# Kernel optimization log

Measured on AMD Instinct MI355X. Metric: run time of the kernel, lower is better.

Reference implementation:

```python
import jax, jax.numpy as jnp
import numpy as np

D_MODEL = 1024
HEADS = 16
Q_DIM = 1024
HEAD_DIM = Q_DIM // HEADS


def setup_inputs() -> dict:
    key = jax.random.key(0)
    ks = jax.random.split(key, 9)
    B, S = 2, 2048
    scale = 1.0 / np.sqrt(D_MODEL)
    inp = {
        "embeddings": jax.random.normal(ks[0], (B, S, D_MODEL), dtype=jnp.float32),
        "Wq": jax.random.normal(ks[1], (D_MODEL, Q_DIM), dtype=jnp.float32) * scale,
        "bq": jnp.zeros((Q_DIM,), dtype=jnp.float32),
        "Wk": jax.random.normal(ks[2], (D_MODEL, Q_DIM), dtype=jnp.float32) * scale,
        "bk": jnp.zeros((Q_DIM,), dtype=jnp.float32),
        "Wv": jax.random.normal(ks[3], (D_MODEL, Q_DIM), dtype=jnp.float32) * scale,
        "bv": jnp.zeros((Q_DIM,), dtype=jnp.float32),
        "Wo": jax.random.normal(ks[4], (Q_DIM, D_MODEL), dtype=jnp.float32) * scale,
        "bo": jnp.zeros((D_MODEL,), dtype=jnp.float32),
    }
    return inp


def reference(embeddings, Wq, bq, Wk, bk, Wv, bv, Wo, bo):
    B, S, _ = embeddings.shape
    # projections -> [B, H, S, Dh]
    def proj(W, b):
        x = embeddings @ W + b
        return x.reshape(B, S, HEADS, HEAD_DIM).transpose(0, 2, 1, 3)
    q = proj(Wq, bq)
    k = proj(Wk, bk)
    v = proj(Wv, bv)
    # scores scaled by sqrt(head_dim) as in source (no mask, dropout is no-op)
    scores = jnp.einsum("bhqd,bhkd->bhqk", q, k) / jnp.sqrt(
        jnp.asarray(HEAD_DIM, dtype=q.dtype)
    )
    p = jax.nn.softmax(scores, axis=-1)
    attn = jnp.einsum("bhqk,bhkd->bhqd", p, v)
    attn = attn.transpose(0, 2, 1, 3).reshape(B, S, Q_DIM)
    return attn @ Wo + bo
```

## Files before the change

kernel.cpp:

```cpp
#include <hip/hip_runtime.h>
#include <hip/hip_bf16.h>

#define BB 2
#define SS 2048
#define DMODEL 1024
#define NHEADS 16
#define DHEAD 64
#define MTOT (BB*SS)
#define NQKV 3072
#define QSCALE 0.18033688011112042f

typedef short bh8 __attribute__((ext_vector_type(8)));
typedef float fx4 __attribute__((ext_vector_type(4)));
typedef unsigned int ux2 __attribute__((ext_vector_type(2)));

__device__ __forceinline__ short f2bs(float f) {
    __hip_bfloat16 h = __float2bfloat16(f);
    return *reinterpret_cast<short*>(&h);
}

__device__ __forceinline__ unsigned pk_bf16(float a, float b) {
    __hip_bfloat162 h = __float22bfloat162_rn(make_float2(a, b));
    return *reinterpret_cast<unsigned*>(&h);
}

__device__ __forceinline__ void gload_lds16(const short* g, short* l) {
    __builtin_amdgcn_global_load_lds(
        (const __attribute__((address_space(1))) unsigned int*)g,
        (__attribute__((address_space(3))) unsigned int*)l, 16, 0, 0);
}

__global__ __launch_bounds__(256) void cvt_emb(const float* __restrict__ x,
                                               short* __restrict__ y, int n) {
    int i = (blockIdx.x * 256 + threadIdx.x) * 4;
    if (i + 3 < n) {
        float4 v = *(const float4*)(x + i);
        short4 o;
        o.x = f2bs(v.x); o.y = f2bs(v.y); o.z = f2bs(v.z); o.w = f2bs(v.w);
        *(short4*)(y + i) = o;
    }
}

__global__ __launch_bounds__(256) void transpose_w(
        const float* __restrict__ Wq, const float* __restrict__ Wk,
        const float* __restrict__ Wv, const float* __restrict__ Wo,
        short* __restrict__ Wt_qkv, short* __restrict__ Wot) {
    __shared__ float tile[64][65];
    int z = blockIdx.z;
    const float* src = (z == 0) ? Wq : (z == 1) ? Wk : (z == 2) ? Wv : Wo;
    short* dst = (z == 3) ? Wot : (Wt_qkv + (size_t)z * 1024 * 1024);
    int n0 = blockIdx.x * 64, k0 = blockIdx.y * 64;
    int tx = threadIdx.x, ty = threadIdx.y;
    for (int j = 0; j < 16; j++) {
        int r = ty + j * 4;
        tile[r][tx] = src[(size_t)(k0 + r) * 1024 + n0 + tx];
    }
    __syncthreads();
    for (int j = 0; j < 16; j++) {
        int r = ty + j * 4;
        dst[(size_t)(n0 + r) * 1024 + k0 + tx] = f2bs(tile[tx][r]);
    }
}

template<int BM, int BN, int NN, int MODE>
__global__ __launch_bounds__(256) void gemm_bt_t(
        const short* __restrict__ A, const short* __restrict__ Bt,
        const float* __restrict__ bq, const float* __restrict__ bk,
        const float* __restrict__ bv, const float* __restrict__ bo,
        short* __restrict__ Qout, short* __restrict__ Kout,
        short* __restrict__ Vtout, float* __restrict__ Cout) {
    const int K = 1024;
    constexpr int ROWS = BM + BN;
    constexpr int CPW  = ROWS / 64;
    constexpr int MBK  = MTOT / BM;
    constexpr int STRIP = MBK / 8;
    constexpr int MT = BM / 32, NT = BN / 32;
    __shared__ __align__(16) short S[3][ROWS * 32];

    int tid = threadIdx.x;
    int w = tid >> 6, l = tid & 63, quad = l >> 4, ln = l & 15;
    int wm = w & 1, wn = w >> 1;

    int id = blockIdx.x;
    int xcd = id & 7, local = id >> 3;
    int mi = xcd * STRIP + (local % STRIP);
    int ni = local / STRIP;
    int m0 = mi * BM, n0 = ni * BN;

    const short* gsrc[CPW];
    int loff[CPW];
    #pragma unroll
    for (int j = 0; j < CPW; j++) {
        int r0 = (w * CPW + j) * 16;
        int row = r0 + (l >> 2);
        gsrc[j] = (r0 < BM ? A + (size_t)(m0 + row) * K
                           : Bt + (size_t)(n0 + row - BM) * K) + (l & 3) * 8;
        loff[j] = r0 * 32;
    }

    short *sC = &S[0][0], *sN = &S[1][0], *sN2 = &S[2][0];
    #pragma unroll
    for (int j = 0; j < CPW; j++) gload_lds16(gsrc[j], sC + loff[j]);
    #pragma unroll
    for (int j = 0; j < CPW; j++) gload_lds16(gsrc[j] + 32, sN + loff[j]);

    fx4 acc[MT][NT] = {};
    for (int it = 0; it < 32; ++it) {
        if (it < 31) {
            if constexpr (CPW == 4)
                asm volatile("s_waitcnt vmcnt(4)\n\ts_barrier" ::: "memory");
            else
                asm volatile("s_waitcnt vmcnt(3)\n\ts_barrier" ::: "memory");
        } else {
            asm volatile("s_waitcnt vmcnt(0)\n\ts_barrier" ::: "memory");
        }
        if (it < 30) {
            int k0 = (it + 2) * 32;
            #pragma unroll
            for (int j = 0; j < CPW; j++) gload_lds16(gsrc[j] + k0, sN2 + loff[j]);
        }
        bh8 af[MT], bf[NT];
        #pragma unroll
        for (int mt = 0; mt < MT; mt++)
            af[mt] = *(const bh8*)&sC[(wm * (BM / 2) + mt * 16 + ln) * 32 + quad * 8];
        #pragma unroll
        for (int nt = 0; nt < NT; nt++)
            bf[nt] = *(const bh8*)&sC[(BM + wn * (BN / 2) + nt * 16 + ln) * 32 + quad * 8];
        #pragma unroll
        for (int mt = 0; mt < MT; mt++)
            #pragma unroll
            for (int nt = 0; nt < NT; nt++)
                acc[mt][nt] = __builtin_amdgcn_mfma_f32_16x16x32_bf16(af[mt], bf[nt], acc[mt][nt], 0, 0, 0);
        short* t;
        t = sC; sC = sN; sN = sN2; sN2 = t;
    }

    #pragma unroll
    for (int mt = 0; mt < MT; mt++) {
        #pragma unroll
        for (int nt = 0; nt < NT; nt++) {
            int n = n0 + wn * (BN / 2) + nt * 16 + ln;
            int mbase = m0 + wm * (BM / 2) + mt * 16 + quad * 4;
            #pragma unroll
            for (int r = 0; r < 4; r++) {
                float v = acc[mt][nt][r];
                int m = mbase + r;
                if constexpr (MODE == 0) {
                    int which = n >> 10, nn = n & 1023, h = nn >> 6, d = nn & 63;
                    float bias = (which == 0) ? bq[nn] : (which == 1) ? bk[nn] : bv[nn];
                    v += bias;
                    int b = m >> 11, s = m & 2047;
                    if (which == 0)
                        Qout[(((size_t)(b * 16 + h) * 2048) + s) * 64 + d] = f2bs(v * QSCALE);
                    else if (which == 1)
                        Kout[(((size_t)(b * 16 + h) * 2048) + s) * 64 + d] = f2bs(v);
                    else
                        Vtout[((size_t)(b * 16 + h) * 64 + d) * 2048 + s] = f2bs(v);
                } else {
                    Cout[(size_t)m * 1024 + n] = v + bo[n];
                }
            }
        }
    }
}

__global__ __launch_bounds__(256, 4) void flash_attn(
        const short* __restrict__ Q, const short* __restrict__ Kg,
        const short* __restrict__ Vt,
        float* __restrict__ O0, float* __restrict__ O1,
        float* __restrict__ L0, float* __restrict__ L1) {
    __shared__ __align__(16) short SH[16384];

    int tid = threadIdx.x;
    int w = tid >> 6, l = tid & 63, quad = l >> 4, ln = l & 15;
    int id = blockIdx.x;
    int xcd = id & 7, local = id >> 3;
    int bh = xcd * 4 + (local & 3);
    int t = local >> 2;
    int qx = t & 15, z = t >> 4;
    int qblk = qx * 128 + w * 32;
    const short* Qb = Q  + (size_t)bh * 2048 * 64;
    const short* Kb = Kg + (size_t)bh * 2048 * 64 + (size_t)z * 1024 * 64;
    const short* Vb = Vt + (size_t)bh * 64 * 2048 + z * 1024;
    float* Op = z ? O1 : O0;
    float* Lp = z ? L1 : L0;
    int swz = ln & 7;

    bh8 qf[2][2];
    #pragma unroll
    for (int qt = 0; qt < 2; qt++)
        #pragma unroll
        for (int c = 0; c < 2; c++)
            qf[qt][c] = *(const bh8*)&Qb[(size_t)(qblk + qt * 16 + ln) * 64 + c * 32 + quad * 8];

    const short* srcK[2]; const short* srcV[2]; int dstoff[2];
    #pragma unroll
    for (int j = 0; j < 2; j++) {
        int c = w * 2 + j;
        int row = c * 8 + (l >> 3);
        int pg = (l & 7) ^ (row & 7);
        srcK[j] = Kb + row * 64 + pg * 8;
        srcV[j] = Vb + (size_t)row * 2048 + pg * 8;
        dstoff[j] = c * 512;
    }

    #pragma unroll
    for (int j = 0; j < 2; j++) {
        gload_lds16(srcK[j], SH + dstoff[j]);
        gload_lds16(srcV[j], SH + 8192 + dstoff[j]);
    }

    fx4 o[2][4] = {};
    float lpart[2] = {0.f, 0.f};

    for (int it = 0; it < 16; ++it) {
        int koff = (it & 1) ? 4096 : 0;
        asm volatile("s_waitcnt vmcnt(0) lgkmcnt(0)\n\ts_barrier" ::: "memory");
        if (it < 15) {
            int noff = koff ^ 4096;
            int kg = (it + 1) * 4096, vg = (it + 1) * 64;
            #pragma unroll
            for (int j = 0; j < 2; j++) {
                gload_lds16(srcK[j] + kg, SH + noff + dstoff[j]);
                gload_lds16(srcV[j] + vg, SH + 8192 + noff + dstoff[j]);
            }
        }
        const short* ksb = SH + koff;
        const short* vsb = SH + 8192 + koff;

        fx4 s[2][4] = {};
        #pragma unroll
        for (int mt = 0; mt < 4; mt++) {
            bh8 kf0 = *(const bh8*)&ksb[(mt * 16 + ln) * 64 + ((quad ^ swz) * 8)];
            bh8 kf1 = *(const bh8*)&ksb[(mt * 16 + ln) * 64 + (((quad + 4) ^ swz) * 8)];
            #pragma unroll
            for (int qt = 0; qt < 2; qt++) {
                s[qt][mt] = __builtin_amdgcn_mfma_f32_16x16x32_bf16(kf0, qf[qt][0], s[qt][mt], 0, 0, 0);
                s[qt][mt] = __builtin_amdgcn_mfma_f32_16x16x32_bf16(kf1, qf[qt][1], s[qt][mt], 0, 0, 0);
            }
        }

        bh8 pf[2][2];
        #pragma unroll
        for (int qt = 0; qt < 2; qt++) {
            float e[4][4];
            #pragma unroll
            for (int mt = 0; mt < 4; mt++) {
                #pragma unroll
                for (int r = 0; r < 4; r++)
                    e[mt][r] = __builtin_amdgcn_exp2f(s[qt][mt][r]);
                lpart[qt] += (e[mt][0] + e[mt][1]) + (e[mt][2] + e[mt][3]);
            }
            #pragma unroll
            for (int c2 = 0; c2 < 2; c2++) {
                unsigned xa = pk_bf16(e[2 * c2][0], e[2 * c2][1]);
                unsigned ya = pk_bf16(e[2 * c2][2], e[2 * c2][3]);
                unsigned xb = pk_bf16(e[2 * c2 + 1][0], e[2 * c2 + 1][1]);
                unsigned yb = pk_bf16(e[2 * c2 + 1][2], e[2 * c2 + 1][3]);
                ux2 u  = __builtin_amdgcn_permlane32_swap(xa, xb, false, false);
                ux2 d02 = __builtin_amdgcn_permlane16_swap(u.x, u.y, false, false);
                ux2 u2 = __builtin_amdgcn_permlane32_swap(ya, yb, false, false);
                ux2 d13 = __builtin_amdgcn_permlane16_swap(u2.x, u2.y, false, false);
                union { unsigned u4[4]; bh8 v; } pk_;
                pk_.u4[0] = d02.x; pk_.u4[1] = d13.x;
                pk_.u4[2] = d02.y; pk_.u4[3] = d13.y;
                pf[qt][c2] = pk_.v;
            }
        }

        #pragma unroll
        for (int c2 = 0; c2 < 2; c2++) {
            #pragma unroll
            for (int dt = 0; dt < 4; dt++) {
                bh8 vf = *(const bh8*)&vsb[(dt * 16 + ln) * 64 + (((c2 * 4 + quad) ^ swz) * 8)];
                o[0][dt] = __builtin_amdgcn_mfma_f32_16x16x32_bf16(vf, pf[0][c2], o[0][dt], 0, 0, 0);
                o[1][dt] = __builtin_amdgcn_mfma_f32_16x16x32_bf16(vf, pf[1][c2], o[1][dt], 0, 0, 0);
            }
        }
    }

    asm volatile("s_waitcnt lgkmcnt(0)\n\ts_barrier" ::: "memory");

    float* PsF = (float*)SH + w * 1088;
    int row = l >> 2, seg = l & 3;
    #pragma unroll
    for (int qt = 0; qt < 2; qt++) {
        #pragma unroll
        for (int dt = 0; dt < 4; dt++)
            *(fx4*)&PsF[ln * 68 + dt * 16 + quad * 4] = o[qt][dt];
        asm volatile("s_waitcnt lgkmcnt(0)" ::: "memory");
        float* orow = &Op[((size_t)bh * 2048 + qblk + qt * 16 + row) * 64];
        #pragma unroll
        for (int j = 0; j < 4; j++) {
            fx4 v = *(fx4*)&PsF[row * 68 + seg * 16 + j * 4];
            *(fx4*)&orow[seg * 16 + j * 4] = v;
        }
        asm volatile("s_waitcnt lgkmcnt(0)" ::: "memory");
        float lr = lpart[qt];
        lr += __shfl_xor(lr, 16);
        lr += __shfl_xor(lr, 32);
        if (l < 16) Lp[(size_t)bh * 2048 + qblk + qt * 16 + l] = lr;
    }
}

__global__ __launch_bounds__(256) void combine(
        const float* __restrict__ O0, const float* __restrict__ O1,
        const float* __restrict__ L0, const float* __restrict__ L1,
        short* __restrict__ Ctx) {
    int t = blockIdx.x * 256 + threadIdx.x;
    size_t base = (size_t)t * 8;
    int bhq = t >> 3;
    int d = (t & 7) * 8;
    int bh = bhq >> 11, q = bhq & 2047;
    int b = bh >> 4, h = bh & 15;
    float inv = 1.0f / (L0[bhq] + L1[bhq]);
    float4 a0 = *(const float4*)(O0 + base);
    float4 a1 = *(const float4*)(O0 + base + 4);
    float4 c0 = *(const float4*)(O1 + base);
    float4 c1 = *(const float4*)(O1 + base + 4);
    union { short s[8]; bh8 v; } o;
    o.s[0] = f2bs((a0.x + c0.x) * inv); o.s[1] = f2bs((a0.y + c0.y) * inv);
    o.s[2] = f2bs((a0.z + c0.z) * inv); o.s[3] = f2bs((a0.w + c0.w) * inv);
    o.s[4] = f2bs((a1.x + c1.x) * inv); o.s[5] = f2bs((a1.y + c1.y) * inv);
    o.s[6] = f2bs((a1.z + c1.z) * inv); o.s[7] = f2bs((a1.w + c1.w) * inv);
    *(bh8*)&Ctx[((size_t)(b * 2048 + q)) * 1024 + h * 64 + d] = o.v;
}

extern "C" void kernel_launch(void* const* d_in, const int* in_sizes, int n_in,
                              void* d_out, int out_size, void* d_ws, size_t ws_size,
                              hipStream_t stream) {
    const float* emb = (const float*)d_in[0];
    const float* Wq  = (const float*)d_in[1];
    const float* bq  = (const float*)d_in[2];
    const float* Wk  = (const float*)d_in[3];
    const float* bk  = (const float*)d_in[4];
    const float* Wv  = (const float*)d_in[5];
    const float* bv  = (const float*)d_in[6];
    const float* Wo  = (const float*)d_in[7];
    const float* bo  = (const float*)d_in[8];

    char* ws = (char*)d_ws;
    const size_t MB = 1024 * 1024;
    short* Xbf  = (short*)(ws + 0);
    short* Wt   = (short*)(ws + 8 * MB);
    float* Op1  = (float*)(ws + 0);
    short* Wot  = (short*)(ws + 17 * MB);
    short* Qb   = (short*)(ws + 19 * MB);
    short* Ctx  = (short*)(ws + 19 * MB);
    short* Kb   = (short*)(ws + 27 * MB);
    short* Vtb  = (short*)(ws + 35 * MB);
    float* L0   = (float*)(ws + 43 * MB);
    float* L1   = (float*)(ws + 43 * MB + 256 * 1024);
    float* Op0  = (float*)d_out;

    cvt_emb<<<4096, 256, 0, stream>>>(emb, Xbf, MTOT * DMODEL);
    transpose_w<<<dim3(16, 16, 4), dim3(64, 4), 0, stream>>>(Wq, Wk, Wv, Wo, Wt, Wot);
    gemm_bt_t<128, 128, NQKV, 0><<<768, 256, 0, stream>>>(
        Xbf, Wt, bq, bk, bv, nullptr, Qb, Kb, Vtb, nullptr);
    flash_attn<<<1024, 256, 0, stream>>>(Qb, Kb, Vtb, Op0, Op1, L0, L1);
    combine<<<2048, 256, 0, stream>>>(Op0, Op1, L0, L1, Ctx);
    gemm_bt_t<64, 128, DMODEL, 1><<<512, 256, 0, stream>>>(
        Ctx, Wot, nullptr, nullptr, nullptr, bo, nullptr, nullptr, nullptr, (float*)d_out);
}
```

Baseline: 208.6 us.

## Drop KV split, fuse combine into flash attention with triple-buffered loads

After: 201.7 us. -3.3%, faster.

```diff
diff --git a/kernel.cpp b/kernel.cpp
--- a/kernel.cpp
+++ b/kernel.cpp
@@ -166,24 +166,20 @@
 
 __global__ __launch_bounds__(256, 4) void flash_attn(
         const short* __restrict__ Q, const short* __restrict__ Kg,
-        const short* __restrict__ Vt,
-        float* __restrict__ O0, float* __restrict__ O1,
-        float* __restrict__ L0, float* __restrict__ L1) {
-    __shared__ __align__(16) short SH[16384];
+        const short* __restrict__ Vt, short* __restrict__ Ctx) {
+    __shared__ __align__(16) short SH[24576];
 
     int tid = threadIdx.x;
     int w = tid >> 6, l = tid & 63, quad = l >> 4, ln = l & 15;
     int id = blockIdx.x;
     int xcd = id & 7, local = id >> 3;
     int bh = xcd * 4 + (local & 3);
-    int t = local >> 2;
-    int qx = t & 15, z = t >> 4;
+    int qx = local >> 2;
     int qblk = qx * 128 + w * 32;
+    int b = bh >> 4, h = bh & 15;
     const short* Qb = Q  + (size_t)bh * 2048 * 64;
-    const short* Kb = Kg + (size_t)bh * 2048 * 64 + (size_t)z * 1024 * 64;
-    const short* Vb = Vt + (size_t)bh * 64 * 2048 + z * 1024;
-    float* Op = z ? O1 : O0;
-    float* Lp = z ? L1 : L0;
+    const short* Kb = Kg + (size_t)bh * 2048 * 64;
+    const short* Vb = Vt + (size_t)bh * 64 * 2048;
     int swz = ln & 7;
 
     bh8 qf[2][2];
@@ -204,29 +200,38 @@
         dstoff[j] = c * 512;
     }
 
+    int kb0 = 0, kb1 = 4096, kb2 = 8192;
+    int vb0 = 12288, vb1 = 16384, vb2 = 20480;
+
     #pragma unroll
     for (int j = 0; j < 2; j++) {
-        gload_lds16(srcK[j], SH + dstoff[j]);
-        gload_lds16(srcV[j], SH + 8192 + dstoff[j]);
+        gload_lds16(srcK[j], SH + kb0 + dstoff[j]);
+        gload_lds16(srcV[j], SH + vb0 + dstoff[j]);
+    }
+    #pragma unroll
+    for (int j = 0; j < 2; j++) {
+        gload_lds16(srcK[j] + 4096, SH + kb1 + dstoff[j]);
+        gload_lds16(srcV[j] + 64,   SH + vb1 + dstoff[j]);
     }
 
     fx4 o[2][4] = {};
     float lpart[2] = {0.f, 0.f};
 
-    for (int it = 0; it < 16; ++it) {
-        int koff = (it & 1) ? 4096 : 0;
-        asm volatile("s_waitcnt vmcnt(0) lgkmcnt(0)\n\ts_barrier" ::: "memory");
-        if (it < 15) {
-            int noff = koff ^ 4096;
-            int kg = (it + 1) * 4096, vg = (it + 1) * 64;
+    for (int it = 0; it < 32; ++it) {
+        if (it < 31)
+            asm volatile("s_waitcnt vmcnt(4) lgkmcnt(0)\n\ts_barrier" ::: "memory");
+        else
+            asm volatile("s_waitcnt vmcnt(0) lgkmcnt(0)\n\ts_barrier" ::: "memory");
+        if (it < 30) {
+            int kg = (it + 2) * 4096, vg = (it + 2) * 64;
             #pragma unroll
             for (int j = 0; j < 2; j++) {
-                gload_lds16(srcK[j] + kg, SH + noff + dstoff[j]);
-                gload_lds16(srcV[j] + vg, SH + 8192 + noff + dstoff[j]);
-            }
-        }
-        const short* ksb = SH + koff;
-        const short* vsb = SH + 8192 + koff;
+                gload_lds16(srcK[j] + kg, SH + kb2 + dstoff[j]);
+                gload_lds16(srcV[j] + vg, SH + vb2 + dstoff[j]);
+            }
+        }
+        const short* ksb = SH + kb0;
+        const short* vsb = SH + vb0;
 
         fx4 s[2][4] = {};
         #pragma unroll
@@ -277,9 +282,13 @@
                 o[1][dt] = __builtin_amdgcn_mfma_f32_16x16x32_bf16(vf, pf[1][c2], o[1][dt], 0, 0, 0);
             }
         }
-    }
-
-    asm volatile("s_waitcnt lgkmcnt(0)\n\ts_barrier" ::: "memory");
+
+        int t0_;
+        t0_ = kb0; kb0 = kb1; kb1 = kb2; kb2 = t0_;
+        t0_ = vb0; vb0 = vb1; vb1 = vb2; vb2 = t0_;
+    }
+
+    asm volatile("s_waitcnt vmcnt(0) lgkmcnt(0)\n\ts_barrier" ::: "memory");
 
     float* PsF = (float*)SH + w * 1088;
     int row = l >> 2, seg = l & 3;
@@ -288,42 +297,34 @@
         #pragma unroll
         for (int dt = 0; dt < 4; dt++)
             *(fx4*)&PsF[ln * 68 + dt * 16 + quad * 4] = o[qt][dt];
-        asm volatile("s_waitcnt lgkmcnt(0)" ::: "memory");
-        float* orow = &Op[((size_t)bh * 2048 + qblk + qt * 16 + row) * 64];
-        #pragma unroll
-        for (int j = 0; j < 4; j++) {
-            fx4 v = *(fx4*)&PsF[row * 68 + seg * 16 + j * 4];
-            *(fx4*)&orow[seg * 16 + j * 4] = v;
-        }
         asm volatile("s_waitcnt lgkmcnt(0)" ::: "memory");
         float lr = lpart[qt];
         lr += __shfl_xor(lr, 16);
         lr += __shfl_xor(lr, 32);
-        if (l < 16) Lp[(size_t)bh * 2048 + qblk + qt * 16 + l] = lr;
-    }
-}
-
-__global__ __launch_bounds__(256) void combine(
-        const float* __restrict__ O0, const float* __restrict__ O1,
-        const float* __restrict__ L0, const float* __restrict__ L1,
-        short* __restrict__ Ctx) {
-    int t = blockIdx.x * 256 + threadIdx.x;
-    size_t base = (size_t)t * 8;
-    int bhq = t >> 3;
-    int d = (t & 7) * 8;
-    int bh = bhq >> 11, q = bhq & 2047;
-    int b = bh >> 4, h = bh & 15;
-    float inv = 1.0f / (L0[bhq] + L1[bhq]);
-    float4 a0 = *(const float4*)(O0 + base);
-    float4 a1 = *(const float4*)(O0 + base + 4);
-    float4 c0 = *(const float4*)(O1 + base);
-    float4 c1 = *(const float4*)(O1 + base + 4);
-    union { short s[8]; bh8 v; } o;
-    o.s[0] = f2bs((a0.x + c0.x) * inv); o.s[1] = f2bs((a0.y + c0.y) * inv);
-    o.s[2] = f2bs((a0.z + c0.z) * inv); o.s[3] = f2bs((a0.w + c0.w) * inv);
-    o.s[4] = f2bs((a1.x + c1.x) * inv); o.s[5] = f2bs((a1.y + c1.y) * inv);
-    o.s[6] = f2bs((a1.z + c1.z) * inv); o.s[7] = f2bs((a1.w + c1.w) * inv);
-    *(bh8*)&Ctx[((size_t)(b * 2048 + q)) * 1024 + h * 64 + d] = o.v;
+        float invr = __shfl(1.0f / lr, row);
+        int q = qblk + qt * 16 + row;
+        short* crow = Ctx + ((size_t)(b * 2048 + q)) * 1024 + h * 64 + seg * 16;
+        union { short s[8]; uint4 u; } o0, o1;
+        #pragma unroll
+        for (int j = 0; j < 2; j++) {
+            fx4 v = *(fx4*)&PsF[row * 68 + seg * 16 + j * 4];
+            o0.s[j * 4 + 0] = f2bs(v[0] * invr);
+            o0.s[j * 4 + 1] = f2bs(v[1] * invr);
+            o0.s[j * 4 + 2] = f2bs(v[2] * invr);
+            o0.s[j * 4 + 3] = f2bs(v[3] * invr);
+        }
+        #pragma unroll
+        for (int j = 2; j < 4; j++) {
+            fx4 v = *(fx4*)&PsF[row * 68 + seg * 16 + j * 4];
+            o1.s[(j - 2) * 4 + 0] = f2bs(v[0] * invr);
+            o1.s[(j - 2) * 4 + 1] = f2bs(v[1] * invr);
+            o1.s[(j - 2) * 4 + 2] = f2bs(v[2] * invr);
+            o1.s[(j - 2) * 4 + 3] = f2bs(v[3] * invr);
+        }
+        *(uint4*)&crow[0] = o0.u;
+        *(uint4*)&crow[8] = o1.u;
+        asm volatile("s_waitcnt lgkmcnt(0)" ::: "memory");
+    }
 }
 
 extern "C" void kernel_launch(void* const* d_in, const int* in_sizes, int n_in,
@@ -342,23 +343,18 @@
     char* ws = (char*)d_ws;
     const size_t MB = 1024 * 1024;
     short* Xbf  = (short*)(ws + 0);
+    short* Ctx  = (short*)(ws + 0);
     short* Wt   = (short*)(ws + 8 * MB);
-    float* Op1  = (float*)(ws + 0);
     short* Wot  = (short*)(ws + 17 * MB);
     short* Qb   = (short*)(ws + 19 * MB);
-    short* Ctx  = (short*)(ws + 19 * MB);
     short* Kb   = (short*)(ws + 27 * MB);
     short* Vtb  = (short*)(ws + 35 * MB);
-    float* L0   = (float*)(ws + 43 * MB);
-    float* L1   = (float*)(ws + 43 * MB + 256 * 1024);
-    float* Op0  = (float*)d_out;
 
     cvt_emb<<<4096, 256, 0, stream>>>(emb, Xbf, MTOT * DMODEL);
     transpose_w<<<dim3(16, 16, 4), dim3(64, 4), 0, stream>>>(Wq, Wk, Wv, Wo, Wt, Wot);
     gemm_bt_t<128, 128, NQKV, 0><<<768, 256, 0, stream>>>(
         Xbf, Wt, bq, bk, bv, nullptr, Qb, Kb, Vtb, nullptr);
-    flash_attn<<<1024, 256, 0, stream>>>(Qb, Kb, Vtb, Op0, Op1, L0, L1);
-    combine<<<2048, 256, 0, stream>>>(Op0, Op1, L0, L1, Ctx);
+    flash_attn<<<512, 256, 0, stream>>>(Qb, Kb, Vtb, Ctx);
     gemm_bt_t<64, 128, DMODEL, 1><<<512, 256, 0, stream>>>(
         Ctx, Wot, nullptr, nullptr, nullptr, bo, nullptr, nullptr, nullptr, (float*)d_out);
 }
```
